# Kernel optimization log

Hardware: AMD Instinct MI355X
Metric: run time of the kernel (lower is better)

The kernel has to match this reference:

```python
import jax, jax.numpy as jnp
import numpy as np

BN_EPS = 1e-5


def setup_inputs() -> dict:
    key = jax.random.key(0)
    ks = jax.random.split(key, 5)
    B, T, N, C, O, K, E = 2, 4, 50000, 32, 32, 3, 800000
    x = jax.random.normal(ks[0], (B, T, N, C), dtype=jnp.float32)
    edge_index = jax.random.randint(ks[1], (2, E), 0, N, dtype=jnp.int64)
    edge_weight = jax.random.uniform(ks[2], (E,), dtype=jnp.float32)
    W = jax.random.normal(ks[3], (K, C, O), dtype=jnp.float32) * 0.05
    bias = jnp.zeros((O,), dtype=jnp.float32)
    gamma = jnp.ones((O,), dtype=jnp.float32)
    beta = jnp.zeros((O,), dtype=jnp.float32)
    return {"x": x, "edge_index": edge_index, "edge_weight": edge_weight,
            "W": W, "bias": bias, "gamma": gamma, "beta": beta}


def reference(x, edge_index, edge_weight, W, bias, gamma, beta):
    # x: [B, T, N, C]; edge_index: [2, E]; W: [K, C, O]
    B, T, N, C = x.shape
    K = W.shape[0]
    src, dst = edge_index[0], edge_index[1]

    # Scaled Laplacian L_hat = 2L/lambda_max - I with sym norm, lambda_max=2
    # => L_hat = -D^{-1/2} A D^{-1/2} (zero diagonal), PyG ChebConv default.
    deg = jax.ops.segment_sum(edge_weight, src, num_segments=N)
    safe = jnp.where(deg > 0, deg, 1.0)
    dinv = jnp.where(deg > 0, 1.0 / jnp.sqrt(safe), 0.0)
    norm = -dinv[src] * edge_weight * dinv[dst]  # [E]

    # Batch all (b, t) slices together: [N, M, C] with M = B*T
    xn = jnp.transpose(x, (2, 0, 1, 3)).reshape(N, B * T, C)

    def lap(z):  # sparse SpMM applied to every (b,t) slice at once
        return jax.ops.segment_sum(norm[:, None, None] * z[src], dst,
                                   num_segments=N)

    # Chebyshev recursion: T0 = x, T1 = L_hat x, Tk = 2 L_hat T_{k-1} - T_{k-2}
    Tx_prev2 = xn
    out = jnp.einsum('nmc,co->nmo', Tx_prev2, W[0])
    if K > 1:
        Tx_prev = lap(xn)
        out = out + jnp.einsum('nmc,co->nmo', Tx_prev, W[1])
        for k in range(2, K):
            Tx_k = 2.0 * lap(Tx_prev) - Tx_prev2
            out = out + jnp.einsum('nmc,co->nmo', Tx_k, W[k])
            Tx_prev2, Tx_prev = Tx_prev, Tx_k
    out = out + bias  # [N, M, O]

    # BatchNorm1d in training mode, applied per (b,t) slice over nodes,
    # exactly as the original per-slice loop does (biased variance).
    mean = jnp.mean(out, axis=0, keepdims=True)              # [1, M, O]
    var = jnp.mean((out - mean) ** 2, axis=0, keepdims=True)  # [1, M, O]
    y = gamma * (out - mean) * jax.lax.rsqrt(var + BN_EPS) + beta
    y = jax.nn.relu(y)

    return jnp.transpose(y.reshape(N, B, T, -1), (1, 2, 0, 3))  # [B,T,N,O]
```

## Files before the change

kernel.cpp:

```cpp
#include <hip/hip_runtime.h>

#define NNODES 50000
#define NEDGES 800000
#define MB 8
#define CF 32
#define OF 32
#define FPN 256
#define TOTAL_OUT (MB * NNODES * OF)
#define NREP 8
#define CAP 64
#define EB (NEDGES / 256)

typedef unsigned short ushort_t;
typedef unsigned int uint_t;
typedef __attribute__((ext_vector_type(8))) short bf16x8;
typedef __attribute__((ext_vector_type(4))) float f32x4;

__device__ __forceinline__ ushort_t f2bf(float f) {
    uint_t u = __float_as_uint(f);
    u += 0x7FFFu + ((u >> 16) & 1u);
    return (ushort_t)(u >> 16);
}
__device__ __forceinline__ float bflo(uint_t u) { return __uint_as_float(u << 16); }
__device__ __forceinline__ float bfhi(uint_t u) { return __uint_as_float(u & 0xFFFF0000u); }

__device__ __forceinline__ bool detect_is64(const int* ei) {
    int lane = threadIdx.x & 63;
    int v = ei[2 * lane + 1];
    return __ballot(v != 0) == 0ULL;
}

__global__ void __launch_bounds__(256) k_build(const int* __restrict__ ei,
                                               const float* __restrict__ w,
                                               const float* __restrict__ x,
                                               float* __restrict__ deg8,
                                               int* __restrict__ counts,
                                               int2* __restrict__ epack,
                                               ushort_t* __restrict__ xn) {
    int b = blockIdx.x;
    int t = threadIdx.x;
    if (b < EB) {
        bool is64 = detect_is64(ei);
        int e = b * 256 + t;
        int s = is64 ? ei[2 * e] : ei[e];
        int d = is64 ? ei[2 * (NEDGES + e)] : ei[NEDGES + e];
        float wt = w[e];
        int rep = b & (NREP - 1);
        atomicAdd(&deg8[s * NREP + rep], wt);
        int pos = atomicAdd(&counts[d], 1);
        if (pos < CAP) {
            int2 pk;
            pk.x = s;
            pk.y = __float_as_int(wt);
            epack[(size_t)d * CAP + pos] = pk;
        }
    } else {
        int bb = b - EB;
        int lane = t & 63;
        int n = bb * 4 + (t >> 6);
        int m = lane >> 3;
        int c = (4 * lane) & 31;
        const float4 v = *(const float4*)(x + ((size_t)m * NNODES + n) * CF + c);
        uint2 d;
        d.x = (uint_t)f2bf(v.x) | ((uint_t)f2bf(v.y) << 16);
        d.y = (uint_t)f2bf(v.z) | ((uint_t)f2bf(v.w) << 16);
        *(uint2*)(xn + (size_t)n * FPN + 4 * lane) = d;
    }
}

__global__ void k_dinv(const float* __restrict__ deg8, float* __restrict__ dinv) {
    int n = blockIdx.x * blockDim.x + threadIdx.x;
    if (n >= NNODES) return;
    const float4* p = (const float4*)(deg8 + (size_t)n * NREP);
    float4 a = p[0], b = p[1];
    float s = a.x + a.y + a.z + a.w + b.x + b.y + b.z + b.w;
    dinv[n] = (s > 0.0f) ? (1.0f / sqrtf(s)) : 0.0f;
}

template <int PHASE>
__global__ void __launch_bounds__(256) k_spmm(const ushort_t* __restrict__ src,
                                              const ushort_t* __restrict__ xn0,
                                              const int* __restrict__ counts,
                                              const int2* __restrict__ epack,
                                              const float* __restrict__ dinv,
                                              ushort_t* __restrict__ dst) {
    int t = threadIdx.x;
    int lane = t & 63;
    int n = __builtin_amdgcn_readfirstlane(blockIdx.x * 4 + (t >> 6));
    int cnt = min(counts[n], CAP);
    float dn = dinv[n];
    float a0 = 0.0f, a1 = 0.0f, a2 = 0.0f, a3 = 0.0f;
    if (cnt > 0) {
        int j = n * CAP + min(lane, cnt - 1);
        int2 ed = epack[j];
        int cv = ed.x;
        float vw = -dinv[cv] * __int_as_float(ed.y) * dn;
        uint_t vv = __float_as_uint(vw);
        for (int k = 0; k < cnt; k += 16) {
            int sc[16]; float v[16];
            #pragma unroll
            for (int i = 0; i < 16; i++) {
                sc[i] = __builtin_amdgcn_readlane(cv, k + i);
                float vr = __uint_as_float(__builtin_amdgcn_readlane((int)vv, k + i));
                v[i] = (k + i < cnt) ? vr : 0.0f;
            }
            uint2 u[16];
            #pragma unroll
            for (int i = 0; i < 16; i++)
                u[i] = *(const uint2*)(src + (size_t)sc[i] * FPN + 4 * lane);
            #pragma unroll
            for (int i = 0; i < 16; i++) {
                a0 += v[i] * bflo(u[i].x);
                a1 += v[i] * bfhi(u[i].x);
                a2 += v[i] * bflo(u[i].y);
                a3 += v[i] * bfhi(u[i].y);
            }
        }
    }
    if (PHASE == 2) {
        const uint2 xu = *(const uint2*)(xn0 + (size_t)n * FPN + 4 * lane);
        a0 = 2.0f * a0 - bflo(xu.x);
        a1 = 2.0f * a1 - bfhi(xu.x);
        a2 = 2.0f * a2 - bflo(xu.y);
        a3 = 2.0f * a3 - bfhi(xu.y);
    }
    uint2 d;
    d.x = (uint_t)f2bf(a0) | ((uint_t)f2bf(a1) << 16);
    d.y = (uint_t)f2bf(a2) | ((uint_t)f2bf(a3) << 16);
    *(uint2*)(dst + (size_t)n * FPN + 4 * lane) = d;
}

__global__ void k_wprep(const float* __restrict__ W, ushort_t* __restrict__ wbf) {
    int tid = threadIdx.x;
    for (int i = tid; i < 384; i += 256) {
        int k    = i >> 7;
        int rem  = i & 127;
        int oh   = rem >> 6;
        int lane = rem & 63;
        int quad = lane >> 4;
        int colc = lane & 15;
        ushort_t* d = wbf + (size_t)i * 8;
        for (int j = 0; j < 8; j++) {
            int c = quad * 8 + j;
            int o = oh * 16 + colc;
            d[j] = f2bf(W[k * (CF * OF) + c * OF + o]);
        }
    }
}

__global__ void __launch_bounds__(256) k_wfuse(const ushort_t* __restrict__ xn,
                                               const ushort_t* __restrict__ t1,
                                               const ushort_t* __restrict__ t2,
                                               const ushort_t* __restrict__ wbf,
                                               const float* __restrict__ bias,
                                               float* __restrict__ out) {
    int t = threadIdx.x;
    int lane = t & 63;
    int wv = blockIdx.x * 4 + (t >> 6);
    if (wv >= NNODES / 16) return;
    int n0 = wv * 16;
    int quad = lane >> 4, col = lane & 15;

    bf16x8 B[6];
    #pragma unroll
    for (int i = 0; i < 6; i++)
        B[i] = *(const bf16x8*)(wbf + (size_t)(i * 64 + lane) * 8);
    float blo = bias[col], bhi = bias[16 + col];

    size_t aoff = (size_t)(n0 + col) * FPN + quad * 8;
    #pragma unroll
    for (int m = 0; m < 8; m++) {
        bf16x8 A0 = *(const bf16x8*)(xn + aoff + m * 32);
        bf16x8 A1 = *(const bf16x8*)(t1 + aoff + m * 32);
        bf16x8 A2 = *(const bf16x8*)(t2 + aoff + m * 32);
        f32x4 lo = { blo, blo, blo, blo };
        f32x4 hi = { bhi, bhi, bhi, bhi };
        lo = __builtin_amdgcn_mfma_f32_16x16x32_bf16(A0, B[0], lo, 0, 0, 0);
        hi = __builtin_amdgcn_mfma_f32_16x16x32_bf16(A0, B[1], hi, 0, 0, 0);
        lo = __builtin_amdgcn_mfma_f32_16x16x32_bf16(A1, B[2], lo, 0, 0, 0);
        hi = __builtin_amdgcn_mfma_f32_16x16x32_bf16(A1, B[3], hi, 0, 0, 0);
        lo = __builtin_amdgcn_mfma_f32_16x16x32_bf16(A2, B[4], lo, 0, 0, 0);
        hi = __builtin_amdgcn_mfma_f32_16x16x32_bf16(A2, B[5], hi, 0, 0, 0);
        float* ob = out + ((size_t)m * NNODES + n0 + quad * 4) * OF + col;
        #pragma unroll
        for (int r = 0; r < 4; r++) {
            ob[(size_t)r * OF]      = lo[r];
            ob[(size_t)r * OF + 16] = hi[r];
        }
    }
}

__global__ void __launch_bounds__(256) k_stats(const float* __restrict__ out,
                                               float* __restrict__ stats) {
    int m = blockIdx.y;
    int t = threadIdx.x;
    int o4 = t & 7, row = t >> 3;
    int n0 = blockIdx.x * 1024;
    int nend = min(n0 + 1024, NNODES);
    float sx = 0, sy = 0, sz = 0, sw = 0;
    float qx = 0, qy = 0, qz = 0, qw = 0;
    for (int n = n0 + row; n < nend; n += 32) {
        const float4 v = *(const float4*)(out + ((size_t)m * NNODES + n) * OF + o4 * 4);
        sx += v.x; sy += v.y; sz += v.z; sw += v.w;
        qx += v.x * v.x; qy += v.y * v.y; qz += v.z * v.z; qw += v.w * v.w;
    }
    __shared__ float4 sS[256];
    __shared__ float4 sQ[256];
    sS[t] = make_float4(sx, sy, sz, sw);
    sQ[t] = make_float4(qx, qy, qz, qw);
    __syncthreads();
    for (int off = 16; off >= 1; off >>= 1) {
        if (row < off) {
            float4 a = sS[t], b = sS[t + off * 8];
            sS[t] = make_float4(a.x + b.x, a.y + b.y, a.z + b.z, a.w + b.w);
            float4 c = sQ[t], d = sQ[t + off * 8];
            sQ[t] = make_float4(c.x + d.x, c.y + d.y, c.z + d.z, c.w + d.w);
        }
        __syncthreads();
    }
    if (row == 0) {
        float4 s = sS[t], q = sQ[t];
        int base = m * 32 + o4 * 4;
        atomicAdd(&stats[base + 0], s.x);
        atomicAdd(&stats[base + 1], s.y);
        atomicAdd(&stats[base + 2], s.z);
        atomicAdd(&stats[base + 3], s.w);
        atomicAdd(&stats[256 + base + 0], q.x);
        atomicAdd(&stats[256 + base + 1], q.y);
        atomicAdd(&stats[256 + base + 2], q.z);
        atomicAdd(&stats[256 + base + 3], q.w);
    }
}

__global__ void __launch_bounds__(256) k_final(float* __restrict__ out,
                                               const float* __restrict__ stats,
                                               const float* __restrict__ gamma,
                                               const float* __restrict__ beta) {
    int idx4 = blockIdx.x * 256 + threadIdx.x;
    size_t base = (size_t)idx4 * 4;
    int o = (int)(base & 31);
    int m = (int)(base / ((size_t)NNODES * OF));
    int mo = m * 32 + o;
    const float4 sm = *(const float4*)(stats + mo);
    const float4 sq = *(const float4*)(stats + 256 + mo);
    const float4 g  = *(const float4*)(gamma + o);
    const float4 bt = *(const float4*)(beta + o);
    const float inv_n = 1.0f / (float)NNODES;
    float4 v = *(const float4*)(out + base);
    {
        float mean = sm.x * inv_n, var = sq.x * inv_n - mean * mean;
        float sc = g.x * rsqrtf(var + 1e-5f);
        v.x = fmaxf(v.x * sc + (bt.x - sc * mean), 0.0f);
    }
    {
        float mean = sm.y * inv_n, var = sq.y * inv_n - mean * mean;
        float sc = g.y * rsqrtf(var + 1e-5f);
        v.y = fmaxf(v.y * sc + (bt.y - sc * mean), 0.0f);
    }
    {
        float mean = sm.z * inv_n, var = sq.z * inv_n - mean * mean;
        float sc = g.z * rsqrtf(var + 1e-5f);
        v.z = fmaxf(v.z * sc + (bt.z - sc * mean), 0.0f);
    }
    {
        float mean = sm.w * inv_n, var = sq.w * inv_n - mean * mean;
        float sc = g.w * rsqrtf(var + 1e-5f);
        v.w = fmaxf(v.w * sc + (bt.w - sc * mean), 0.0f);
    }
    *(float4*)(out + base) = v;
}

extern "C" void kernel_launch(void* const* d_in, const int* in_sizes, int n_in,
                              void* d_out, int out_size, void* d_ws, size_t ws_size,
                              hipStream_t stream) {
    const float* x     = (const float*)d_in[0];
    const int*   ei    = (const int*)d_in[1];
    const float* w     = (const float*)d_in[2];
    const float* W     = (const float*)d_in[3];
    const float* bias  = (const float*)d_in[4];
    const float* gamma = (const float*)d_in[5];
    const float* beta  = (const float*)d_in[6];
    float* out = (float*)d_out;

    char* p = (char*)d_ws;
    auto alloc = [&](size_t bytes) {
        char* r = p;
        p += (bytes + 511) & ~(size_t)511;
        return r;
    };
    int*      counts = (int*)alloc((size_t)NNODES * 4);
    float*    deg8   = (float*)alloc((size_t)NNODES * NREP * 4);
    float*    stats  = (float*)alloc(512 * 4);
    float*    dinv   = (float*)alloc((size_t)NNODES * 4);
    int2*     epack  = (int2*)alloc((size_t)NNODES * CAP * 8);
    ushort_t* wbf    = (ushort_t*)alloc(384 * 8 * 2);
    ushort_t* xn     = (ushort_t*)alloc((size_t)NNODES * FPN * 2);
    ushort_t* t1     = (ushort_t*)alloc((size_t)NNODES * FPN * 2);
    ushort_t* t2     = (ushort_t*)alloc((size_t)NNODES * FPN * 2);

    size_t zlen = (char*)(stats + 512) - (char*)counts;
    hipMemsetAsync(counts, 0, zlen, stream);

    k_wprep<<<1, 256, 0, stream>>>(W, wbf);
    k_build<<<EB + NNODES / 4, 256, 0, stream>>>(ei, w, x, deg8, counts, epack, xn);
    k_dinv<<<(NNODES + 255) / 256, 256, 0, stream>>>(deg8, dinv);

    k_spmm<1><<<NNODES / 4, 256, 0, stream>>>(xn, xn, counts, epack, dinv, t1);
    k_spmm<2><<<NNODES / 4, 256, 0, stream>>>(t1, xn, counts, epack, dinv, t2);

    int wfblocks = (NNODES / 16 + 3) / 4;
    k_wfuse<<<wfblocks, 256, 0, stream>>>(xn, t1, t2, wbf, bias, out);

    dim3 sgrid((NNODES + 1023) / 1024, MB);
    k_stats<<<sgrid, 256, 0, stream>>>(out, stats);
    k_final<<<TOTAL_OUT / 4 / 256, 256, 0, stream>>>(out, stats, gamma, beta);
}
```

Measured before the change: 367.9 us.

## Switch feature layout to slice-major and precompute normalized edge weights

Intermediate bf16 feature buffers change from node-major with all 8 slices interleaved to slice-major [M][N][32]. The SpMM is rewritten so each block handles one slice for 32 nodes with 8 lanes per node, which shrinks the per-slice gather footprint and should improve cache locality. A new k_norm pass folds the dinv scaling into epack weights ahead of time, so both SpMM phases skip the dinv gathers. The W prep and dinv kernels are merged into one launch. The cost is more gather requests per edge, each only 64 bytes wide, and an extra kernel launch.

```diff
diff --git a/kernel.cpp b/kernel.cpp
--- a/kernel.cpp
+++ b/kernel.cpp
@@ -5,11 +5,11 @@
 #define MB 8
 #define CF 32
 #define OF 32
-#define FPN 256
 #define TOTAL_OUT (MB * NNODES * OF)
 #define NREP 8
 #define CAP 64
 #define EB (NEDGES / 256)
+#define CVB (TOTAL_OUT / (256 * 8))
 
 typedef unsigned short ushort_t;
 typedef unsigned int uint_t;
@@ -55,26 +55,61 @@
             epack[(size_t)d * CAP + pos] = pk;
         }
     } else {
-        int bb = b - EB;
-        int lane = t & 63;
-        int n = bb * 4 + (t >> 6);
-        int m = lane >> 3;
-        int c = (4 * lane) & 31;
-        const float4 v = *(const float4*)(x + ((size_t)m * NNODES + n) * CF + c);
-        uint2 d;
-        d.x = (uint_t)f2bf(v.x) | ((uint_t)f2bf(v.y) << 16);
-        d.y = (uint_t)f2bf(v.z) | ((uint_t)f2bf(v.w) << 16);
-        *(uint2*)(xn + (size_t)n * FPN + 4 * lane) = d;
-    }
-}
-
-__global__ void k_dinv(const float* __restrict__ deg8, float* __restrict__ dinv) {
-    int n = blockIdx.x * blockDim.x + threadIdx.x;
-    if (n >= NNODES) return;
-    const float4* p = (const float4*)(deg8 + (size_t)n * NREP);
-    float4 a = p[0], b = p[1];
-    float s = a.x + a.y + a.z + a.w + b.x + b.y + b.z + b.w;
-    dinv[n] = (s > 0.0f) ? (1.0f / sqrtf(s)) : 0.0f;
+        size_t idx = (size_t)(b - EB) * 256 + t;
+        const float4* xp = (const float4*)x + idx * 2;
+        float4 v0 = xp[0], v1 = xp[1];
+        uint4 dd;
+        dd.x = (uint_t)f2bf(v0.x) | ((uint_t)f2bf(v0.y) << 16);
+        dd.y = (uint_t)f2bf(v0.z) | ((uint_t)f2bf(v0.w) << 16);
+        dd.z = (uint_t)f2bf(v1.x) | ((uint_t)f2bf(v1.y) << 16);
+        dd.w = (uint_t)f2bf(v1.z) | ((uint_t)f2bf(v1.w) << 16);
+        *(uint4*)(xn + idx * 8) = dd;
+    }
+}
+
+__global__ void k_dinv_wprep(const float* __restrict__ deg8, float* __restrict__ dinv,
+                             const float* __restrict__ W, ushort_t* __restrict__ wbf) {
+    if (blockIdx.x < 196) {
+        int n = blockIdx.x * blockDim.x + threadIdx.x;
+        if (n >= NNODES) return;
+        const float4* p = (const float4*)(deg8 + (size_t)n * NREP);
+        float4 a = p[0], b = p[1];
+        float s = a.x + a.y + a.z + a.w + b.x + b.y + b.z + b.w;
+        dinv[n] = (s > 0.0f) ? (1.0f / sqrtf(s)) : 0.0f;
+    } else {
+        int tid = threadIdx.x;
+        for (int i = tid; i < 384; i += 256) {
+            int k    = i >> 7;
+            int rem  = i & 127;
+            int oh   = rem >> 6;
+            int lane = rem & 63;
+            int quad = lane >> 4;
+            int colc = lane & 15;
+            ushort_t* d = wbf + (size_t)i * 8;
+            for (int j = 0; j < 8; j++) {
+                int c = quad * 8 + j;
+                int o = oh * 16 + colc;
+                d[j] = f2bf(W[k * (CF * OF) + c * OF + o]);
+            }
+        }
+    }
+}
+
+__global__ void __launch_bounds__(256) k_norm(int* __restrict__ counts,
+                                              int2* __restrict__ epack,
+                                              const float* __restrict__ dinv) {
+    int t = threadIdx.x;
+    int lane = t & 63;
+    int n = blockIdx.x * 4 + (t >> 6);
+    int cnt = min(counts[n], CAP);
+    float dn = dinv[n];
+    if (lane < cnt) {
+        size_t idx = (size_t)n * CAP + lane;
+        int2 ed = epack[idx];
+        float vw = -dinv[ed.x] * __int_as_float(ed.y) * dn;
+        epack[idx].y = __float_as_int(vw);
+    }
+    if (lane == 0) counts[n] = cnt;
 }
 
 template <int PHASE>
@@ -82,43 +117,40 @@
                                               const ushort_t* __restrict__ xn0,
                                               const int* __restrict__ counts,
                                               const int2* __restrict__ epack,
-                                              const float* __restrict__ dinv,
                                               ushort_t* __restrict__ dst) {
     int t = threadIdx.x;
-    int lane = t & 63;
-    int n = __builtin_amdgcn_readfirstlane(blockIdx.x * 4 + (t >> 6));
-    int cnt = min(counts[n], CAP);
-    float dn = dinv[n];
+    int p = blockIdx.x & 7;
+    int g = blockIdx.x >> 3;
+    int n = g * 32 + (t >> 3);
+    int l = t & 7;
+    if (n >= NNODES) return;
+    int cnt = counts[n];
+    const ushort_t* sp = src + (size_t)p * NNODES * 32;
     float a0 = 0.0f, a1 = 0.0f, a2 = 0.0f, a3 = 0.0f;
-    if (cnt > 0) {
-        int j = n * CAP + min(lane, cnt - 1);
-        int2 ed = epack[j];
-        int cv = ed.x;
-        float vw = -dinv[cv] * __int_as_float(ed.y) * dn;
-        uint_t vv = __float_as_uint(vw);
-        for (int k = 0; k < cnt; k += 16) {
-            int sc[16]; float v[16];
-            #pragma unroll
-            for (int i = 0; i < 16; i++) {
-                sc[i] = __builtin_amdgcn_readlane(cv, k + i);
-                float vr = __uint_as_float(__builtin_amdgcn_readlane((int)vv, k + i));
-                v[i] = (k + i < cnt) ? vr : 0.0f;
-            }
-            uint2 u[16];
-            #pragma unroll
-            for (int i = 0; i < 16; i++)
-                u[i] = *(const uint2*)(src + (size_t)sc[i] * FPN + 4 * lane);
-            #pragma unroll
-            for (int i = 0; i < 16; i++) {
-                a0 += v[i] * bflo(u[i].x);
-                a1 += v[i] * bfhi(u[i].x);
-                a2 += v[i] * bflo(u[i].y);
-                a3 += v[i] * bfhi(u[i].y);
-            }
-        }
-    }
+    for (int k = 0; k < cnt; k += 16) {
+        int2 ed[16];
+        #pragma unroll
+        for (int i = 0; i < 16; i++) {
+            int idx = min(k + i, cnt - 1);
+            ed[i] = epack[(size_t)n * CAP + idx];
+            if (k + i >= cnt) ed[i].y = 0;
+        }
+        uint2 u[16];
+        #pragma unroll
+        for (int i = 0; i < 16; i++)
+            u[i] = *(const uint2*)(sp + (size_t)ed[i].x * 32 + l * 4);
+        #pragma unroll
+        for (int i = 0; i < 16; i++) {
+            float vw = __int_as_float(ed[i].y);
+            a0 += vw * bflo(u[i].x);
+            a1 += vw * bfhi(u[i].x);
+            a2 += vw * bflo(u[i].y);
+            a3 += vw * bfhi(u[i].y);
+        }
+    }
+    size_t off = ((size_t)p * NNODES + n) * 32 + l * 4;
     if (PHASE == 2) {
-        const uint2 xu = *(const uint2*)(xn0 + (size_t)n * FPN + 4 * lane);
+        const uint2 xu = *(const uint2*)(xn0 + off);
         a0 = 2.0f * a0 - bflo(xu.x);
         a1 = 2.0f * a1 - bfhi(xu.x);
         a2 = 2.0f * a2 - bflo(xu.y);
@@ -127,25 +159,7 @@
     uint2 d;
     d.x = (uint_t)f2bf(a0) | ((uint_t)f2bf(a1) << 16);
     d.y = (uint_t)f2bf(a2) | ((uint_t)f2bf(a3) << 16);
-    *(uint2*)(dst + (size_t)n * FPN + 4 * lane) = d;
-}
-
-__global__ void k_wprep(const float* __restrict__ W, ushort_t* __restrict__ wbf) {
-    int tid = threadIdx.x;
-    for (int i = tid; i < 384; i += 256) {
-        int k    = i >> 7;
-        int rem  = i & 127;
-        int oh   = rem >> 6;
-        int lane = rem & 63;
-        int quad = lane >> 4;
-        int colc = lane & 15;
-        ushort_t* d = wbf + (size_t)i * 8;
-        for (int j = 0; j < 8; j++) {
-            int c = quad * 8 + j;
-            int o = oh * 16 + colc;
-            d[j] = f2bf(W[k * (CF * OF) + c * OF + o]);
-        }
-    }
+    *(uint2*)(dst + off) = d;
 }
 
 __global__ void __launch_bounds__(256) k_wfuse(const ushort_t* __restrict__ xn,
@@ -167,12 +181,12 @@
         B[i] = *(const bf16x8*)(wbf + (size_t)(i * 64 + lane) * 8);
     float blo = bias[col], bhi = bias[16 + col];
 
-    size_t aoff = (size_t)(n0 + col) * FPN + quad * 8;
     #pragma unroll
     for (int m = 0; m < 8; m++) {
-        bf16x8 A0 = *(const bf16x8*)(xn + aoff + m * 32);
-        bf16x8 A1 = *(const bf16x8*)(t1 + aoff + m * 32);
-        bf16x8 A2 = *(const bf16x8*)(t2 + aoff + m * 32);
+        size_t aoff = ((size_t)m * NNODES + n0 + col) * 32 + quad * 8;
+        bf16x8 A0 = *(const bf16x8*)(xn + aoff);
+        bf16x8 A1 = *(const bf16x8*)(t1 + aoff);
+        bf16x8 A2 = *(const bf16x8*)(t2 + aoff);
         f32x4 lo = { blo, blo, blo, blo };
         f32x4 hi = { bhi, bhi, bhi, bhi };
         lo = __builtin_amdgcn_mfma_f32_16x16x32_bf16(A0, B[0], lo, 0, 0, 0);
@@ -294,19 +308,20 @@
     float*    dinv   = (float*)alloc((size_t)NNODES * 4);
     int2*     epack  = (int2*)alloc((size_t)NNODES * CAP * 8);
     ushort_t* wbf    = (ushort_t*)alloc(384 * 8 * 2);
-    ushort_t* xn     = (ushort_t*)alloc((size_t)NNODES * FPN * 2);
-    ushort_t* t1     = (ushort_t*)alloc((size_t)NNODES * FPN * 2);
-    ushort_t* t2     = (ushort_t*)alloc((size_t)NNODES * FPN * 2);
+    ushort_t* xn     = (ushort_t*)alloc((size_t)TOTAL_OUT * 2);
+    ushort_t* t1     = (ushort_t*)alloc((size_t)TOTAL_OUT * 2);
+    ushort_t* t2     = (ushort_t*)alloc((size_t)TOTAL_OUT * 2);
 
     size_t zlen = (char*)(stats + 512) - (char*)counts;
     hipMemsetAsync(counts, 0, zlen, stream);
 
-    k_wprep<<<1, 256, 0, stream>>>(W, wbf);
-    k_build<<<EB + NNODES / 4, 256, 0, stream>>>(ei, w, x, deg8, counts, epack, xn);
-    k_dinv<<<(NNODES + 255) / 256, 256, 0, stream>>>(deg8, dinv);
-
-    k_spmm<1><<<NNODES / 4, 256, 0, stream>>>(xn, xn, counts, epack, dinv, t1);
-    k_spmm<2><<<NNODES / 4, 256, 0, stream>>>(t1, xn, counts, epack, dinv, t2);
+    k_build<<<EB + CVB, 256, 0, stream>>>(ei, w, x, deg8, counts, epack, xn);
+    k_dinv_wprep<<<197, 256, 0, stream>>>(deg8, dinv, W, wbf);
+    k_norm<<<NNODES / 4, 256, 0, stream>>>(counts, epack, dinv);
+
+    int ng = (NNODES + 31) / 32;
+    k_spmm<1><<<ng * 8, 256, 0, stream>>>(xn, xn, counts, epack, t1);
+    k_spmm<2><<<ng * 8, 256, 0, stream>>>(t1, xn, counts, epack, t2);
 
     int wfblocks = (NNODES / 16 + 3) / 4;
     k_wfuse<<<wfblocks, 256, 0, stream>>>(xn, t1, t2, wbf, bias, out);
```

After: 440.0 us. 19.6% more time.
